# Kernel tuning notes

Measured on AMD Instinct MI355X. Metric: run time of the kernel, lower is better.

Reference implementation:

```python
import jax, jax.numpy as jnp
import numpy as np

NEG_INF = -1e30  # stand-in for float('-inf'); avoids inf-inf NaN edge cases, same softmax result


def setup_inputs() -> dict:
    key = jax.random.key(0)
    k1, k2, k3, k4, k5 = jax.random.split(key, 5)
    B, T, C, H = 16, 2048, 200, 64
    x = jax.random.normal(k1, (B, T, C), dtype=jnp.float32)
    # padding mask over key positions, broadcastable to [B, T, T]
    padding_mask = jax.random.randint(k2, (B, 1, T), 0, 2, dtype=jnp.int32)
    # nn.Linear(n_embd, head_size, bias=False) weights, stored as [C, H] so y = x @ W
    Wk = jax.random.normal(k3, (C, H), dtype=jnp.float32) * (C ** -0.5)
    Wq = jax.random.normal(k4, (C, H), dtype=jnp.float32) * (C ** -0.5)
    Wv = jax.random.normal(k5, (C, H), dtype=jnp.float32) * (C ** -0.5)
    return {"x": x, "padding_mask": padding_mask, "Wk": Wk, "Wq": Wq, "Wv": Wv}


def reference(x, padding_mask, Wk, Wq, Wv):
    # x: [B,T,C]; padding_mask: [B,1,T] (0 = padded key position)
    k = x @ Wk  # [B,T,H]
    q = x @ Wq  # [B,T,H]
    v = x @ Wv  # [B,T,H]
    scale = k.shape[-1] ** -0.5
    wei = jnp.einsum("bqh,bkh->bqk", q, k) * scale  # [B,T,T]
    # mask padded key columns before softmax
    wei = jnp.where(padding_mask == 0, NEG_INF, wei)
    wei = jax.nn.softmax(wei, axis=-1)
    # mask padded query rows (transpose of padding mask) to exact zero after softmax
    mask_t = jnp.swapaxes(padding_mask, -2, -1)  # [B,T,1]
    wei = jnp.where(mask_t == 0, 0.0, wei)
    # dropout is identity in eval mode
    out = jnp.einsum("bqk,bkh->bqh", wei, v)  # [B,T,H]
    return out
```

## Files before the change

### kernel.cpp

```cpp
#include <hip/hip_runtime.h>


typedef __attribute__((ext_vector_type(8))) __bf16 bf16x8;
typedef __attribute__((ext_vector_type(4))) __bf16 bf16x4;
typedef __attribute__((ext_vector_type(4))) float f32x4;

#define T_SEQ 2048
#define C_DIM 200
#define H_DIM 64
#define BT_TOT 32768
#define QKV_ELEMS 2097152
#define PPAD 72
#define OPAD 68
#define WTF_FULL 36864
#define WTF_ELEMS 38400
#define LOG2E 1.44269504088896f

__global__ void prep_w(const float* __restrict__ Wk, const float* __restrict__ Wq,
                       const float* __restrict__ Wv, __bf16* __restrict__ WtF) {
    int idx = blockIdx.x * 256 + threadIdx.x;
    if (idx >= WTF_ELEMS) return;
    int w, c, h;
    if (idx < WTF_FULL) {
        int j = idx & 7, lane = (idx >> 3) & 63;
        int chunk = idx >> 9;
        int t = chunk & 3, rest = chunk >> 2;
        w = rest % 3; int ks = rest / 3;
        c = ks * 32 + (lane >> 4) * 8 + j;
        h = t * 16 + (lane & 15);
    } else {
        int i2 = idx - WTF_FULL;
        int j = i2 & 7, l15 = (i2 >> 3) & 15, t = (i2 >> 7) & 3;
        w = i2 >> 9;
        c = 192 + j;
        h = t * 16 + l15;
    }
    const float* W = (w == 0) ? Wq : (w == 1) ? Wk : Wv;
    float val = W[c * H_DIM + h];
    if (w == 0) val *= 0.125f * LOG2E;
    WtF[idx] = (__bf16)val;
}

__global__ __launch_bounds__(256) void qkv_proj(const float* __restrict__ x,
                                                const __bf16* __restrict__ WtF,
                                                __bf16* __restrict__ qb,
                                                __bf16* __restrict__ kb,
                                                __bf16* __restrict__ vT) {
    __shared__ __bf16 Wl[19200];

    const int tid = threadIdx.x;
    const int wave = tid >> 6, lane = tid & 63, l15 = lane & 15, quad = lane >> 4;
    const int rt = blockIdx.x >> 1;
    const int hh = blockIdx.x & 1;
    const int m0b = rt * 64;
    const int row0 = m0b + wave * 16;

    f32x4 acc[3][2] = {};

    #pragma unroll
    for (int i = 0; i < 10; ++i) {
        const int u = i * 256 + tid;
        if (u < 2400) {
            int src;
            if (u < 2304) {
                const int lc = u >> 6, off = u & 63;
                const int ks = lc / 6, r6 = lc % 6;
                const int w = r6 >> 1, tt = r6 & 1;
                src = ((ks * 12 + w * 4 + 2 * hh + tt) << 6) + off;
            } else {
                const int u2 = u - 2304;
                const int w = u2 >> 5, tt = (u2 >> 4) & 1, un = u2 & 15;
                src = (WTF_FULL >> 3) + ((w * 4 + 2 * hh + tt) << 4) + un;
            }
            *(bf16x8*)(Wl + u * 8) = *(const bf16x8*)(WtF + src * 8);
        }
    }
    __syncthreads();

    #pragma unroll
    for (int ks = 0; ks < 7; ++ks) {
        bf16x8 a;
        if (ks < 6 || quad == 0) {
            const float* xr = x + (size_t)(row0 + l15) * C_DIM + ks * 32 + quad * 8;
            const float4 f0 = *(const float4*)xr;
            const float4 f1 = *(const float4*)(xr + 4);
            a[0]=(__bf16)f0.x; a[1]=(__bf16)f0.y; a[2]=(__bf16)f0.z; a[3]=(__bf16)f0.w;
            a[4]=(__bf16)f1.x; a[5]=(__bf16)f1.y; a[6]=(__bf16)f1.z; a[7]=(__bf16)f1.w;
        } else {
            #pragma unroll
            for (int j = 0; j < 8; ++j) a[j] = (__bf16)0.f;
        }
        #pragma unroll
        for (int w = 0; w < 3; ++w)
            #pragma unroll
            for (int tt = 0; tt < 2; ++tt) {
                const int off = (ks < 6) ? (((ks * 6 + w * 2 + tt) << 9) + lane * 8)
                                         : (18432 + ((w * 2 + tt) << 7) + l15 * 8);
                const bf16x8 bf = *(const bf16x8*)(Wl + off);
                acc[w][tt] = __builtin_amdgcn_mfma_f32_16x16x32_bf16(a, bf, acc[w][tt], 0, 0, 0);
            }
    }

    #pragma unroll
    for (int tt = 0; tt < 2; ++tt)
        #pragma unroll
        for (int r = 0; r < 4; ++r) {
            const size_t m = row0 + quad * 4 + r;
            const int h = hh * 32 + tt * 16 + l15;
            qb[m * H_DIM + h] = (__bf16)acc[0][tt][r];
            kb[m * H_DIM + h] = (__bf16)acc[1][tt][r];
        }
    __syncthreads();
    #pragma unroll
    for (int tt = 0; tt < 2; ++tt)
        #pragma unroll
        for (int r = 0; r < 4; ++r)
            Wl[(tt * 16 + l15) * 72 + wave * 16 + quad * 4 + r] = (__bf16)acc[2][tt][r];
    __syncthreads();
    const int bb = m0b >> 11, tloc = m0b & 2047;
    {
        const int seg = tid;
        const int hl = seg >> 3, s8 = seg & 7;
        *(bf16x8*)(vT + ((size_t)bb * H_DIM + hh * 32 + hl) * T_SEQ + tloc + s8 * 8) =
            *(const bf16x8*)(Wl + hl * 72 + s8 * 8);
    }
}

__global__ __launch_bounds__(256, 2) void attn(const __bf16* __restrict__ qb,
                                               const __bf16* __restrict__ kb,
                                               const __bf16* __restrict__ vT,
                                               const int* __restrict__ pm,
                                               float* __restrict__ out) {
    __shared__ __align__(16) char arena[8192 + 36864];
    float* biasS = (float*)arena;

    const int tid = threadIdx.x;
    const int wave = tid >> 6, lane = tid & 63, l15 = lane & 15, quad = lane >> 4;
    const int ks = wave;
    const int b = blockIdx.y;
    const int q0 = blockIdx.x * 64;
    const size_t bT = (size_t)b * T_SEQ;

    for (int i = tid; i < 512; i += 256) {
        const int4 p4 = *(const int4*)(pm + bT + i * 4);
        biasS[i * 4 + 0] = p4.x ? 0.f : -1e30f;
        biasS[i * 4 + 1] = p4.y ? 0.f : -1e30f;
        biasS[i * 4 + 2] = p4.z ? 0.f : -1e30f;
        biasS[i * 4 + 3] = p4.w ? 0.f : -1e30f;
    }
    __syncthreads();

    bf16x8 qa[4][2];
    #pragma unroll
    for (int mt = 0; mt < 4; ++mt)
        #pragma unroll
        for (int s = 0; s < 2; ++s)
            qa[mt][s] = *(const bf16x8*)(qb + (bT + q0 + mt * 16 + l15) * H_DIM + s * 32 + quad * 8);

    __bf16* P = (__bf16*)(arena + 8192) + wave * (64 * PPAD);
    const __bf16* kbase = kb + bT * H_DIM;
    const __bf16* vbase = vT + (size_t)b * H_DIM * T_SEQ;

    f32x4 oacc[4][4] = {};
    float lsum[4] = {0.f, 0.f, 0.f, 0.f};

    bf16x8 kf[8];
    bf16x8 vf[8];
    #pragma unroll
    for (int n = 0; n < 4; ++n)
        #pragma unroll
        for (int s = 0; s < 2; ++s)
            kf[n * 2 + s] = *(const bf16x8*)(kbase + (ks * 512 + n * 16 + l15) * H_DIM + s * 32 + quad * 8);
    #pragma unroll
    for (int t = 0; t < 4; ++t)
        #pragma unroll
        for (int s = 0; s < 2; ++s)
            vf[t * 2 + s] = *(const bf16x8*)(vbase + (size_t)(t * 16 + l15) * T_SEQ + ks * 512 + s * 32 + quad * 8);

    for (int kt = 0; kt < 8; ++kt) {
        const int key0 = ks * 512 + kt * 64;
        const int keyn = ks * 512 + ((kt < 7) ? kt + 1 : 7) * 64;

        bf16x8 pa[4][2];

        #pragma unroll
        for (int n = 0; n < 2; ++n) {
            const f32x4 bias = *(const f32x4*)(biasS + key0 + n * 16 + quad * 4);
            f32x4 s_[4];
            #pragma unroll
            for (int mt = 0; mt < 4; ++mt) s_[mt] = bias;
            __builtin_amdgcn_s_setprio(1);
            #pragma unroll
            for (int s = 0; s < 2; ++s)
                #pragma unroll
                for (int mt = 0; mt < 4; ++mt)
                    s_[mt] = __builtin_amdgcn_mfma_f32_16x16x32_bf16(kf[n * 2 + s], qa[mt][s], s_[mt], 0, 0, 0);
            __builtin_amdgcn_s_setprio(0);
            #pragma unroll
            for (int mt = 0; mt < 4; ++mt) {
                bf16x4 p4;
                #pragma unroll
                for (int r = 0; r < 4; ++r) {
                    const float e = exp2f(s_[mt][r]);
                    lsum[mt] += e;
                    p4[r] = (__bf16)e;
                }
                *(bf16x4*)(P + (mt * 16 + l15) * PPAD + n * 16 + quad * 4) = p4;
            }
        }
        #pragma unroll
        for (int mt = 0; mt < 4; ++mt)
            pa[mt][0] = *(const bf16x8*)(P + (mt * 16 + l15) * PPAD + quad * 8);

        #pragma unroll
        for (int n = 2; n < 4; ++n) {
            const f32x4 bias = *(const f32x4*)(biasS + key0 + n * 16 + quad * 4);
            f32x4 s_[4];
            #pragma unroll
            for (int mt = 0; mt < 4; ++mt) s_[mt] = bias;
            __builtin_amdgcn_s_setprio(1);
            #pragma unroll
            for (int s = 0; s < 2; ++s)
                #pragma unroll
                for (int mt = 0; mt < 4; ++mt)
                    s_[mt] = __builtin_amdgcn_mfma_f32_16x16x32_bf16(kf[n * 2 + s], qa[mt][s], s_[mt], 0, 0, 0);
            __builtin_amdgcn_s_setprio(0);
            #pragma unroll
            for (int mt = 0; mt < 4; ++mt) {
                bf16x4 p4;
                #pragma unroll
                for (int r = 0; r < 4; ++r) {
                    const float e = exp2f(s_[mt][r]);
                    lsum[mt] += e;
                    p4[r] = (__bf16)e;
                }
                *(bf16x4*)(P + (mt * 16 + l15) * PPAD + n * 16 + quad * 4) = p4;
            }
        }
        #pragma unroll
        for (int mt = 0; mt < 4; ++mt)
            pa[mt][1] = *(const bf16x8*)(P + (mt * 16 + l15) * PPAD + 32 + quad * 8);

        #pragma unroll
        for (int n = 0; n < 4; ++n)
            #pragma unroll
            for (int s = 0; s < 2; ++s)
                kf[n * 2 + s] = *(const bf16x8*)(kbase + (keyn + n * 16 + l15) * H_DIM + s * 32 + quad * 8);

        __builtin_amdgcn_s_setprio(1);
        #pragma unroll
        for (int t = 0; t < 4; ++t)
            #pragma unroll
            for (int mt = 0; mt < 4; ++mt)
                oacc[mt][t] = __builtin_amdgcn_mfma_f32_16x16x32_bf16(pa[mt][0], vf[t * 2 + 0], oacc[mt][t], 0, 0, 0);

        #pragma unroll
        for (int t = 0; t < 4; ++t)
            #pragma unroll
            for (int mt = 0; mt < 4; ++mt)
                oacc[mt][t] = __builtin_amdgcn_mfma_f32_16x16x32_bf16(pa[mt][1], vf[t * 2 + 1], oacc[mt][t], 0, 0, 0);
        __builtin_amdgcn_s_setprio(0);

        if (kt < 7) {
            #pragma unroll
            for (int t = 0; t < 4; ++t)
                #pragma unroll
                for (int s = 0; s < 2; ++s)
                    vf[t * 2 + s] = *(const bf16x8*)(vbase + (size_t)(t * 16 + l15) * T_SEQ + keyn + s * 32 + quad * 8);
        }
    }

    #pragma unroll
    for (int mt = 0; mt < 4; ++mt) {
        lsum[mt] += __shfl_xor(lsum[mt], 16, 64);
        lsum[mt] += __shfl_xor(lsum[mt], 32, 64);
    }

    float* Ocomb = (float*)(arena + 8192);
    float* Lcomb = Ocomb + 64 * OPAD;

    __syncthreads();
    if (ks == 1) {
        #pragma unroll
        for (int mt = 0; mt < 4; ++mt) {
            #pragma unroll
            for (int t = 0; t < 4; ++t)
                #pragma unroll
                for (int r = 0; r < 4; ++r)
                    Ocomb[(mt * 16 + quad * 4 + r) * OPAD + t * 16 + l15] = oacc[mt][t][r];
            if (quad == 0) Lcomb[mt * 16 + l15] = lsum[mt];
        }
    }
    __syncthreads();
    if (ks == 2) {
        #pragma unroll
        for (int mt = 0; mt < 4; ++mt) {
            #pragma unroll
            for (int t = 0; t < 4; ++t)
                #pragma unroll
                for (int r = 0; r < 4; ++r)
                    Ocomb[(mt * 16 + quad * 4 + r) * OPAD + t * 16 + l15] += oacc[mt][t][r];
            if (quad == 0) Lcomb[mt * 16 + l15] += lsum[mt];
        }
    }
    __syncthreads();
    if (ks == 3) {
        #pragma unroll
        for (int mt = 0; mt < 4; ++mt) {
            #pragma unroll
            for (int t = 0; t < 4; ++t)
                #pragma unroll
                for (int r = 0; r < 4; ++r)
                    Ocomb[(mt * 16 + quad * 4 + r) * OPAD + t * 16 + l15] += oacc[mt][t][r];
            if (quad == 0) Lcomb[mt * 16 + l15] += lsum[mt];
        }
    }
    __syncthreads();
    if (ks == 0) {
        #pragma unroll
        for (int mt = 0; mt < 4; ++mt) {
            lsum[mt] += Lcomb[mt * 16 + l15];
            #pragma unroll
            for (int t = 0; t < 4; ++t)
                #pragma unroll
                for (int r = 0; r < 4; ++r)
                    oacc[mt][t][r] += Ocomb[(mt * 16 + quad * 4 + r) * OPAD + t * 16 + l15];
            #pragma unroll
            for (int r = 0; r < 4; ++r) {
                const int qpos = q0 + mt * 16 + quad * 4 + r;
                const float lv = __shfl(lsum[mt], quad * 4 + r, 64);
                const bool qvalid = biasS[qpos] == 0.f;
                const float inv = (qvalid && lv > 0.f) ? 1.f / lv : 0.f;
                #pragma unroll
                for (int t = 0; t < 4; ++t)
                    out[(bT + qpos) * H_DIM + t * 16 + l15] = oacc[mt][t][r] * inv;
            }
        }
    }
}

extern "C" void kernel_launch(void* const* d_in, const int* in_sizes, int n_in,
                              void* d_out, int out_size, void* d_ws, size_t ws_size,
                              hipStream_t stream) {
    const float* x  = (const float*)d_in[0];
    const int* pm   = (const int*)d_in[1];
    const float* Wk = (const float*)d_in[2];
    const float* Wq = (const float*)d_in[3];
    const float* Wv = (const float*)d_in[4];
    float* out = (float*)d_out;

    __bf16* qb  = (__bf16*)d_ws;
    __bf16* kb  = qb + QKV_ELEMS;
    __bf16* vT  = kb + QKV_ELEMS;
    __bf16* WtF = vT + QKV_ELEMS;

    prep_w<<<dim3((WTF_ELEMS + 255) / 256), dim3(256), 0, stream>>>(Wk, Wq, Wv, WtF);
    qkv_proj<<<dim3(BT_TOT / 64 * 2), dim3(256), 0, stream>>>(x, WtF, qb, kb, vT);
    attn<<<dim3(T_SEQ / 64, 16), dim3(256), 0, stream>>>(qb, kb, vT, pm, out);
}
```

Measured before the change: 126.7 us.

## Software-pipeline attention loop: overlap next QK^T MFMA with current softmax exp

Restructures the per-wave key loop into 32-key half-steps with double-buffered K/V fragments and score accumulators. The QK^T MFMAs for the next half-tile are issued while the exp2/convert/LDS-write of the current half-tile runs, so matrix and vector work can overlap. The P staging buffer shrinks to 32 columns, cutting LDS use. In exchange it needs more registers for the double buffers and drops the s_setprio hints, which may raise register pressure or spill at the two-blocks-per-CU launch bound.

```diff
diff --git a/kernel.cpp b/kernel.cpp
--- a/kernel.cpp
+++ b/kernel.cpp
@@ -10,7 +10,7 @@
 #define H_DIM 64
 #define BT_TOT 32768
 #define QKV_ELEMS 2097152
-#define PPAD 72
+#define PPAD2 36
 #define OPAD 68
 #define WTF_FULL 36864
 #define WTF_ELEMS 38400
@@ -126,12 +126,95 @@
     }
 }
 
+template <int CUR, bool DO_QK, bool DO_PREF>
+__device__ __forceinline__ void attn_body(
+    int h, int kW, int l15, int quad,
+    const float* __restrict__ biasS, __bf16* __restrict__ P,
+    const __bf16* __restrict__ kbase, const __bf16* __restrict__ vbase,
+    bf16x8 (&qa)[4][2], bf16x8 (&kf)[2][4], bf16x8 (&vf)[2][4],
+    f32x4 (&sb)[2][4][2], f32x4 (&oacc)[4][4], float (&lsum)[4]) {
+    constexpr int NXT = CUR ^ 1;
+
+    if (DO_PREF) {
+        #pragma unroll
+        for (int n = 0; n < 2; ++n)
+            #pragma unroll
+            for (int s = 0; s < 2; ++s)
+                kf[CUR][n * 2 + s] = *(const bf16x8*)(kbase +
+                    (size_t)(kW + (h + 2) * 32 + n * 16 + l15) * H_DIM + s * 32 + quad * 8);
+    }
+
+    if (DO_QK) {
+        const f32x4 b0 = *(const f32x4*)(biasS + kW + (h + 1) * 32 + quad * 4);
+        #pragma unroll
+        for (int mt = 0; mt < 4; ++mt) sb[NXT][mt][0] = b0;
+        #pragma unroll
+        for (int s = 0; s < 2; ++s)
+            #pragma unroll
+            for (int mt = 0; mt < 4; ++mt)
+                sb[NXT][mt][0] = __builtin_amdgcn_mfma_f32_16x16x32_bf16(
+                    kf[NXT][s], qa[mt][s], sb[NXT][mt][0], 0, 0, 0);
+    }
+    #pragma unroll
+    for (int mt = 0; mt < 4; ++mt) {
+        bf16x4 p4;
+        #pragma unroll
+        for (int r = 0; r < 4; ++r) {
+            const float e = exp2f(sb[CUR][mt][0][r]);
+            lsum[mt] += e;
+            p4[r] = (__bf16)e;
+        }
+        *(bf16x4*)(P + (mt * 16 + l15) * PPAD2 + quad * 4) = p4;
+    }
+    if (DO_QK) {
+        const f32x4 b1 = *(const f32x4*)(biasS + kW + (h + 1) * 32 + 16 + quad * 4);
+        #pragma unroll
+        for (int mt = 0; mt < 4; ++mt) sb[NXT][mt][1] = b1;
+        #pragma unroll
+        for (int s = 0; s < 2; ++s)
+            #pragma unroll
+            for (int mt = 0; mt < 4; ++mt)
+                sb[NXT][mt][1] = __builtin_amdgcn_mfma_f32_16x16x32_bf16(
+                    kf[NXT][2 + s], qa[mt][s], sb[NXT][mt][1], 0, 0, 0);
+    }
+    #pragma unroll
+    for (int mt = 0; mt < 4; ++mt) {
+        bf16x4 p4;
+        #pragma unroll
+        for (int r = 0; r < 4; ++r) {
+            const float e = exp2f(sb[CUR][mt][1][r]);
+            lsum[mt] += e;
+            p4[r] = (__bf16)e;
+        }
+        *(bf16x4*)(P + (mt * 16 + l15) * PPAD2 + 16 + quad * 4) = p4;
+    }
+
+    bf16x8 pa[4];
+    #pragma unroll
+    for (int mt = 0; mt < 4; ++mt)
+        pa[mt] = *(const bf16x8*)(P + (mt * 16 + l15) * PPAD2 + quad * 8);
+
+    #pragma unroll
+    for (int t = 0; t < 4; ++t)
+        #pragma unroll
+        for (int mt = 0; mt < 4; ++mt)
+            oacc[mt][t] = __builtin_amdgcn_mfma_f32_16x16x32_bf16(
+                pa[mt], vf[CUR][t], oacc[mt][t], 0, 0, 0);
+
+    if (DO_PREF) {
+        #pragma unroll
+        for (int t = 0; t < 4; ++t)
+            vf[CUR][t] = *(const bf16x8*)(vbase +
+                (size_t)(t * 16 + l15) * T_SEQ + kW + (h + 2) * 32 + quad * 8);
+    }
+}
+
 __global__ __launch_bounds__(256, 2) void attn(const __bf16* __restrict__ qb,
                                                const __bf16* __restrict__ kb,
                                                const __bf16* __restrict__ vT,
                                                const int* __restrict__ pm,
                                                float* __restrict__ out) {
-    __shared__ __align__(16) char arena[8192 + 36864];
+    __shared__ __align__(16) char arena[8192 + 4 * 64 * PPAD2 * 2];
     float* biasS = (float*)arena;
 
     const int tid = threadIdx.x;
@@ -157,118 +240,54 @@
         for (int s = 0; s < 2; ++s)
             qa[mt][s] = *(const bf16x8*)(qb + (bT + q0 + mt * 16 + l15) * H_DIM + s * 32 + quad * 8);
 
-    __bf16* P = (__bf16*)(arena + 8192) + wave * (64 * PPAD);
+    __bf16* P = (__bf16*)(arena + 8192) + wave * (64 * PPAD2);
     const __bf16* kbase = kb + bT * H_DIM;
     const __bf16* vbase = vT + (size_t)b * H_DIM * T_SEQ;
+    const int kW = ks * 512;
 
     f32x4 oacc[4][4] = {};
     float lsum[4] = {0.f, 0.f, 0.f, 0.f};
 
-    bf16x8 kf[8];
-    bf16x8 vf[8];
-    #pragma unroll
-    for (int n = 0; n < 4; ++n)
+    bf16x8 kf[2][4];
+    bf16x8 vf[2][4];
+    f32x4 sb[2][4][2];
+
+    #pragma unroll
+    for (int hp = 0; hp < 2; ++hp) {
+        #pragma unroll
+        for (int n = 0; n < 2; ++n)
+            #pragma unroll
+            for (int s = 0; s < 2; ++s)
+                kf[hp][n * 2 + s] = *(const bf16x8*)(kbase +
+                    (size_t)(kW + hp * 32 + n * 16 + l15) * H_DIM + s * 32 + quad * 8);
+        #pragma unroll
+        for (int t = 0; t < 4; ++t)
+            vf[hp][t] = *(const bf16x8*)(vbase + (size_t)(t * 16 + l15) * T_SEQ + kW + hp * 32 + quad * 8);
+    }
+    #pragma unroll
+    for (int n = 0; n < 2; ++n) {
+        const f32x4 b0 = *(const f32x4*)(biasS + kW + n * 16 + quad * 4);
+        #pragma unroll
+        for (int mt = 0; mt < 4; ++mt) sb[0][mt][n] = b0;
         #pragma unroll
         for (int s = 0; s < 2; ++s)
-            kf[n * 2 + s] = *(const bf16x8*)(kbase + (ks * 512 + n * 16 + l15) * H_DIM + s * 32 + quad * 8);
-    #pragma unroll
-    for (int t = 0; t < 4; ++t)
-        #pragma unroll
-        for (int s = 0; s < 2; ++s)
-            vf[t * 2 + s] = *(const bf16x8*)(vbase + (size_t)(t * 16 + l15) * T_SEQ + ks * 512 + s * 32 + quad * 8);
-
-    for (int kt = 0; kt < 8; ++kt) {
-        const int key0 = ks * 512 + kt * 64;
-        const int keyn = ks * 512 + ((kt < 7) ? kt + 1 : 7) * 64;
-
-        bf16x8 pa[4][2];
-
-        #pragma unroll
-        for (int n = 0; n < 2; ++n) {
-            const f32x4 bias = *(const f32x4*)(biasS + key0 + n * 16 + quad * 4);
-            f32x4 s_[4];
-            #pragma unroll
-            for (int mt = 0; mt < 4; ++mt) s_[mt] = bias;
-            __builtin_amdgcn_s_setprio(1);
-            #pragma unroll
-            for (int s = 0; s < 2; ++s)
-                #pragma unroll
-                for (int mt = 0; mt < 4; ++mt)
-                    s_[mt] = __builtin_amdgcn_mfma_f32_16x16x32_bf16(kf[n * 2 + s], qa[mt][s], s_[mt], 0, 0, 0);
-            __builtin_amdgcn_s_setprio(0);
-            #pragma unroll
-            for (int mt = 0; mt < 4; ++mt) {
-                bf16x4 p4;
-                #pragma unroll
-                for (int r = 0; r < 4; ++r) {
-                    const float e = exp2f(s_[mt][r]);
-                    lsum[mt] += e;
-                    p4[r] = (__bf16)e;
-                }
-                *(bf16x4*)(P + (mt * 16 + l15) * PPAD + n * 16 + quad * 4) = p4;
-            }
-        }
-        #pragma unroll
-        for (int mt = 0; mt < 4; ++mt)
-            pa[mt][0] = *(const bf16x8*)(P + (mt * 16 + l15) * PPAD + quad * 8);
-
-        #pragma unroll
-        for (int n = 2; n < 4; ++n) {
-            const f32x4 bias = *(const f32x4*)(biasS + key0 + n * 16 + quad * 4);
-            f32x4 s_[4];
-            #pragma unroll
-            for (int mt = 0; mt < 4; ++mt) s_[mt] = bias;
-            __builtin_amdgcn_s_setprio(1);
-            #pragma unroll
-            for (int s = 0; s < 2; ++s)
-                #pragma unroll
-                for (int mt = 0; mt < 4; ++mt)
-                    s_[mt] = __builtin_amdgcn_mfma_f32_16x16x32_bf16(kf[n * 2 + s], qa[mt][s], s_[mt], 0, 0, 0);
-            __builtin_amdgcn_s_setprio(0);
-            #pragma unroll
-            for (int mt = 0; mt < 4; ++mt) {
-                bf16x4 p4;
-                #pragma unroll
-                for (int r = 0; r < 4; ++r) {
-                    const float e = exp2f(s_[mt][r]);
-                    lsum[mt] += e;
-                    p4[r] = (__bf16)e;
-                }
-                *(bf16x4*)(P + (mt * 16 + l15) * PPAD + n * 16 + quad * 4) = p4;
-            }
-        }
-        #pragma unroll
-        for (int mt = 0; mt < 4; ++mt)
-            pa[mt][1] = *(const bf16x8*)(P + (mt * 16 + l15) * PPAD + 32 + quad * 8);
-
-        #pragma unroll
-        for (int n = 0; n < 4; ++n)
-            #pragma unroll
-            for (int s = 0; s < 2; ++s)
-                kf[n * 2 + s] = *(const bf16x8*)(kbase + (keyn + n * 16 + l15) * H_DIM + s * 32 + quad * 8);
-
-        __builtin_amdgcn_s_setprio(1);
-        #pragma unroll
-        for (int t = 0; t < 4; ++t)
             #pragma unroll
             for (int mt = 0; mt < 4; ++mt)
-                oacc[mt][t] = __builtin_amdgcn_mfma_f32_16x16x32_bf16(pa[mt][0], vf[t * 2 + 0], oacc[mt][t], 0, 0, 0);
-
-        #pragma unroll
-        for (int t = 0; t < 4; ++t)
-            #pragma unroll
-            for (int mt = 0; mt < 4; ++mt)
-                oacc[mt][t] = __builtin_amdgcn_mfma_f32_16x16x32_bf16(pa[mt][1], vf[t * 2 + 1], oacc[mt][t], 0, 0, 0);
-        __builtin_amdgcn_s_setprio(0);
-
-        if (kt < 7) {
-            #pragma unroll
-            for (int t = 0; t < 4; ++t)
-                #pragma unroll
-                for (int s = 0; s < 2; ++s)
-                    vf[t * 2 + s] = *(const bf16x8*)(vbase + (size_t)(t * 16 + l15) * T_SEQ + keyn + s * 32 + quad * 8);
-        }
-    }
+                sb[0][mt][n] = __builtin_amdgcn_mfma_f32_16x16x32_bf16(
+                    kf[0][n * 2 + s], qa[mt][s], sb[0][mt][n], 0, 0, 0);
+    }
+
+    for (int kt = 0; kt < 7; ++kt) {
+        const int h0 = kt * 2;
+        attn_body<0, true, true>(h0, kW, l15, quad, biasS, P, kbase, vbase,
+                                 qa, kf, vf, sb, oacc, lsum);
+        attn_body<1, true, true>(h0 + 1, kW, l15, quad, biasS, P, kbase, vbase,
+                                 qa, kf, vf, sb, oacc, lsum);
+    }
+    attn_body<0, true, false>(14, kW, l15, quad, biasS, P, kbase, vbase,
+                              qa, kf, vf, sb, oacc, lsum);
+    attn_body<1, false, false>(15, kW, l15, quad, biasS, P, kbase, vbase,
+                               qa, kf, vf, sb, oacc, lsum);
 
     #pragma unroll
     for (int mt = 0; mt < 4; ++mt) {
```

New measurement: 136.0 us. 1.07x slower.

## Remap blocks per XCD by batch and simplify attention loop pipelining

Applied to the files above, without the earlier changes.

Blocks are remapped so that each XCD (selected by flat block id mod 8) works on only two batches, which is meant to improve L2 reuse of that batch's K/V. Inside the loop, V is now loaded at the start of each iteration instead of being prefetched one iteration ahead. The split two-phase QK/softmax with early P reads is merged into one loop, and the s_setprio hints are removed. This cuts register pressure, but V load latency is exposed within the iteration and the QK and PV overlap is lost.

```diff
diff --git a/kernel.cpp b/kernel.cpp
--- a/kernel.cpp
+++ b/kernel.cpp
@@ -137,8 +137,11 @@
     const int tid = threadIdx.x;
     const int wave = tid >> 6, lane = tid & 63, l15 = lane & 15, quad = lane >> 4;
     const int ks = wave;
-    const int b = blockIdx.y;
-    const int q0 = blockIdx.x * 64;
+
+    const int flat = blockIdx.y * 32 + blockIdx.x;
+    const int xcd = flat & 7, j = flat >> 3;
+    const int b = xcd + 8 * (j & 1);
+    const int q0 = (j >> 1) * 64;
     const size_t bT = (size_t)b * T_SEQ;
 
     for (int i = tid; i < 512; i += 256) {
@@ -165,37 +168,33 @@
     float lsum[4] = {0.f, 0.f, 0.f, 0.f};
 
     bf16x8 kf[8];
-    bf16x8 vf[8];
     #pragma unroll
     for (int n = 0; n < 4; ++n)
         #pragma unroll
         for (int s = 0; s < 2; ++s)
             kf[n * 2 + s] = *(const bf16x8*)(kbase + (ks * 512 + n * 16 + l15) * H_DIM + s * 32 + quad * 8);
-    #pragma unroll
-    for (int t = 0; t < 4; ++t)
-        #pragma unroll
-        for (int s = 0; s < 2; ++s)
-            vf[t * 2 + s] = *(const bf16x8*)(vbase + (size_t)(t * 16 + l15) * T_SEQ + ks * 512 + s * 32 + quad * 8);
 
     for (int kt = 0; kt < 8; ++kt) {
         const int key0 = ks * 512 + kt * 64;
-        const int keyn = ks * 512 + ((kt < 7) ? kt + 1 : 7) * 64;
-
-        bf16x8 pa[4][2];
-
-        #pragma unroll
-        for (int n = 0; n < 2; ++n) {
+
+        bf16x8 vf[8];
+        #pragma unroll
+        for (int t = 0; t < 4; ++t)
+            #pragma unroll
+            for (int s = 0; s < 2; ++s)
+                vf[t * 2 + s] = *(const bf16x8*)(vbase + (size_t)(t * 16 + l15) * T_SEQ + key0 + s * 32 + quad * 8);
+
+        #pragma unroll
+        for (int n = 0; n < 4; ++n) {
             const f32x4 bias = *(const f32x4*)(biasS + key0 + n * 16 + quad * 4);
             f32x4 s_[4];
             #pragma unroll
             for (int mt = 0; mt < 4; ++mt) s_[mt] = bias;
-            __builtin_amdgcn_s_setprio(1);
             #pragma unroll
             for (int s = 0; s < 2; ++s)
                 #pragma unroll
                 for (int mt = 0; mt < 4; ++mt)
                     s_[mt] = __builtin_amdgcn_mfma_f32_16x16x32_bf16(kf[n * 2 + s], qa[mt][s], s_[mt], 0, 0, 0);
-            __builtin_amdgcn_s_setprio(0);
             #pragma unroll
             for (int mt = 0; mt < 4; ++mt) {
                 bf16x4 p4;
@@ -208,66 +207,28 @@
                 *(bf16x4*)(P + (mt * 16 + l15) * PPAD + n * 16 + quad * 4) = p4;
             }
         }
+
+        const int keyn = ks * 512 + ((kt < 7) ? kt + 1 : 7) * 64;
+        #pragma unroll
+        for (int n = 0; n < 4; ++n)
+            #pragma unroll
+            for (int s = 0; s < 2; ++s)
+                kf[n * 2 + s] = *(const bf16x8*)(kbase + (keyn + n * 16 + l15) * H_DIM + s * 32 + quad * 8);
+
+        bf16x8 pa[4][2];
         #pragma unroll
         for (int mt = 0; mt < 4; ++mt)
-            pa[mt][0] = *(const bf16x8*)(P + (mt * 16 + l15) * PPAD + quad * 8);
-
-        #pragma unroll
-        for (int n = 2; n < 4; ++n) {
-            const f32x4 bias = *(const f32x4*)(biasS + key0 + n * 16 + quad * 4);
-            f32x4 s_[4];
-            #pragma unroll
-            for (int mt = 0; mt < 4; ++mt) s_[mt] = bias;
-            __builtin_amdgcn_s_setprio(1);
+            #pragma unroll
+            for (int s = 0; s < 2; ++s)
+                pa[mt][s] = *(const bf16x8*)(P + (mt * 16 + l15) * PPAD + s * 32 + quad * 8);
+
+        #pragma unroll
+        for (int t = 0; t < 4; ++t)
             #pragma unroll
             for (int s = 0; s < 2; ++s)
                 #pragma unroll
                 for (int mt = 0; mt < 4; ++mt)
-                    s_[mt] = __builtin_amdgcn_mfma_f32_16x16x32_bf16(kf[n * 2 + s], qa[mt][s], s_[mt], 0, 0, 0);
-            __builtin_amdgcn_s_setprio(0);
-            #pragma unroll
-            for (int mt = 0; mt < 4; ++mt) {
-                bf16x4 p4;
-                #pragma unroll
-                for (int r = 0; r < 4; ++r) {
-                    const float e = exp2f(s_[mt][r]);
-                    lsum[mt] += e;
-                    p4[r] = (__bf16)e;
-                }
-                *(bf16x4*)(P + (mt * 16 + l15) * PPAD + n * 16 + quad * 4) = p4;
-            }
-        }
-        #pragma unroll
-        for (int mt = 0; mt < 4; ++mt)
-            pa[mt][1] = *(const bf16x8*)(P + (mt * 16 + l15) * PPAD + 32 + quad * 8);
-
-        #pragma unroll
-        for (int n = 0; n < 4; ++n)
-            #pragma unroll
-            for (int s = 0; s < 2; ++s)
-                kf[n * 2 + s] = *(const bf16x8*)(kbase + (keyn + n * 16 + l15) * H_DIM + s * 32 + quad * 8);
-
-        __builtin_amdgcn_s_setprio(1);
-        #pragma unroll
-        for (int t = 0; t < 4; ++t)
-            #pragma unroll
-            for (int mt = 0; mt < 4; ++mt)
-                oacc[mt][t] = __builtin_amdgcn_mfma_f32_16x16x32_bf16(pa[mt][0], vf[t * 2 + 0], oacc[mt][t], 0, 0, 0);
-
-        #pragma unroll
-        for (int t = 0; t < 4; ++t)
-            #pragma unroll
-            for (int mt = 0; mt < 4; ++mt)
-                oacc[mt][t] = __builtin_amdgcn_mfma_f32_16x16x32_bf16(pa[mt][1], vf[t * 2 + 1], oacc[mt][t], 0, 0, 0);
-        __builtin_amdgcn_s_setprio(0);
-
-        if (kt < 7) {
-            #pragma unroll
-            for (int t = 0; t < 4; ++t)
-                #pragma unroll
-                for (int s = 0; s < 2; ++s)
-                    vf[t * 2 + s] = *(const bf16x8*)(vbase + (size_t)(t * 16 + l15) * T_SEQ + keyn + s * 32 + quad * 8);
-        }
+                    oacc[mt][t] = __builtin_amdgcn_mfma_f32_16x16x32_bf16(pa[mt][s], vf[t * 2 + s], oacc[mt][t], 0, 0, 0);
     }
 
     #pragma unroll
```

Result: no change. 127.0 us (+0.2%).
